# Kernel optimization log

Measured on AMD Instinct MI355X. Metric: run time of the kernel, lower is better.

## Reference

```python
import jax, jax.numpy as jnp
import numpy as np

B, N = 2, 6
FC, FH, FW = 256, 32, 88            # encoder feature shape
ORFH, ORFW = 256, 704               # original image H, W
OUT_C = 128
D_ST, D_END, D_STEP = 1.0, 60.0, 3.0
NXV, NYV, NZV = 256, 256, 1         # BEV voxel grid (x, y, z)
DXV = np.array([0.4, 0.4, 20.0], np.float32)          # dx
BXV = np.array([-51.0, -51.0, 0.0], np.float32)       # bx = bound_lo + dx/2
BN_EPS = 1e-3


def _conv(x, w, b):
    y = jax.lax.conv_general_dilated(x, w, (1, 1), 'SAME',
                                     dimension_numbers=('NCHW', 'OIHW', 'NCHW'))
    return y + b[None, :, None, None]


def _bn(x, scale, bias, mean, var):
    inv = scale / jnp.sqrt(var + BN_EPS)
    return x * inv[None, :, None, None] + (bias - mean * inv)[None, :, None, None]


def _frustum():
    ds = jnp.arange(D_ST, D_END, D_STEP, dtype=jnp.float32)      # (D,)
    xs = jnp.linspace(0.0, ORFW - 1.0, FW)
    ys = jnp.linspace(0.0, ORFH - 1.0, FH)
    f = jnp.stack(jnp.broadcast_arrays(xs[None, None, :], ys[None, :, None],
                                       ds[:, None, None]), axis=-1)  # (D,FH,FW,3)
    return f, ds


def _forward(cam2ego_rot, cam2ego_trans, cam_intrins, post_cam2ego_rot,
             post_cam2ego_trans, img_feats,
             conv1_w, conv1_b, bn1_s, bn1_b, bn1_m, bn1_v,
             conv2_w, conv2_b, bn2_s, bn2_b, bn2_m, bn2_v,
             conv3_w, conv3_b):
    frustum, depth_vals = _frustum()
    D = depth_vals.shape[0]
    # ---- geometry (GaussianLSS.get_geometry) ----
    pts = frustum[None, None] - post_cam2ego_trans[:, :, None, None, None, :]
    inv_post = jnp.linalg.inv(post_cam2ego_rot)                       # (B,N,3,3)
    pts = jnp.einsum('bnij,bndhwj->bndhwi', inv_post, pts)
    pts = jnp.concatenate([pts[..., :2] * pts[..., 2:3], pts[..., 2:3]], -1)
    combine = cam2ego_rot @ jnp.linalg.inv(cam_intrins)
    geometry = (jnp.einsum('bnij,bndhwj->bndhwi', combine, pts)
                + cam2ego_trans[:, :, None, None, None, :])           # (B,N,D,H,W,3)
    # ---- depth net + gaussian depth distribution (get_cam_feature) ----
    x = img_feats.reshape(B * N, FC, FH, FW)
    x = jax.nn.relu(_bn(_conv(x, conv1_w, conv1_b), bn1_s, bn1_b, bn1_m, bn1_v))
    x = jax.nn.relu(_bn(_conv(x, conv2_w, conv2_b), bn2_s, bn2_b, bn2_m, bn2_v))
    x = _conv(x, conv3_w, conv3_b)                                    # (BN, OUT_C+2, H, W)
    mu, log_sigma, feats = x[:, 0], x[:, 1], x[:, 2:]
    sigma = jnp.exp(log_sigma) + 1e-6
    g = jnp.exp(-0.5 * (depth_vals[None, :, None, None] - mu[:, None]) ** 2
                / (sigma[:, None] ** 2))                              # (BN,D,H,W)
    g = g / (jnp.sum(g, axis=1, keepdims=True) + 1e-6)
    vol = g[:, None] * feats[:, :, None]                              # (BN,C,D,H,W)
    vol = vol.reshape(B, N, OUT_C, D, FH, FW).transpose(0, 1, 3, 4, 5, 2)  # (B,N,D,H,W,C)
    # ---- bev_pool: voxelize + scatter-add ----
    dx = jnp.asarray(DXV)
    bx = jnp.asarray(BXV)
    geom = ((geometry - (bx - dx / 2.0)) / dx).astype(jnp.int32)      # trunc like .long()
    gx, gy, gz = geom[..., 0], geom[..., 1], geom[..., 2]
    kept = ((gx >= 0) & (gx < NXV) & (gy >= 0) & (gy < NYV)
            & (gz >= 0) & (gz < NZV))                                 # (B,N,D,H,W)
    bidx = jnp.arange(B, dtype=jnp.int32)[:, None, None, None, None]
    flat = ((bidx * NZV + gz) * NXV + gx) * NYV + gy
    flat = jnp.where(kept, flat, 0)
    w = kept.astype(vol.dtype)
    data = (vol * w[..., None]).reshape(-1, OUT_C)
    bev = jax.ops.segment_sum(data, flat.reshape(-1),
                              num_segments=B * NZV * NXV * NYV)
    # torch: (B,C,Z,X,Y) -> cat(unbind(dim=2), 1) -> (B, Z*C, X, Y)
    bev = bev.reshape(B, NZV, NXV, NYV, OUT_C).transpose(0, 1, 4, 2, 3)
    bev = bev.reshape(B, NZV * OUT_C, NXV, NYV)
    # ---- ref_bev_pool mask ----
    counts = jax.ops.segment_sum(w.reshape(-1), flat.reshape(-1),
                                 num_segments=B * NZV * NXV * NYV)
    mask = jnp.any(counts.reshape(B, NZV, NXV, NYV) > 0, axis=1)      # (B,X,Y) bool
    return bev, mask


def setup_inputs() -> dict:
    key = jax.random.key(0)
    ks = jax.random.split(key, 16)
    # camera->ego rotation: cam z -> ego x, cam x -> -ego y, cam y -> -ego z
    R = jnp.array([[0., 0., 1.], [-1., 0., 0.], [0., -1., 0.]], jnp.float32)
    cam2ego_rot = jnp.tile(R, (B, N, 1, 1)) + 0.01 * jax.random.normal(ks[0], (B, N, 3, 3))
    cam2ego_trans = jax.random.uniform(ks[1], (B, N, 3), minval=-2.0, maxval=2.0)
    K = jnp.array([[500., 0., ORFW / 2.], [0., 500., ORFH / 2.], [0., 0., 1.]], jnp.float32)
    cam_intrins = jnp.tile(K, (B, N, 1, 1))
    post_cam2ego_rot = jnp.tile(jnp.eye(3, dtype=jnp.float32), (B, N, 1, 1)) \
        + 0.005 * jax.random.normal(ks[2], (B, N, 3, 3))
    post_cam2ego_trans = 0.5 * jax.random.normal(ks[3], (B, N, 3))
    img_feats = 0.1 * jax.random.normal(ks[4], (B, N, FC, FH, FW))
    conv3_b = jnp.zeros((OUT_C + 2,)).at[0].set(25.0).at[1].set(2.3)  # mu~25m, sigma~10m
    return dict(
        cam2ego_rot=cam2ego_rot, cam2ego_trans=cam2ego_trans,
        cam_intrins=cam_intrins, post_cam2ego_rot=post_cam2ego_rot,
        post_cam2ego_trans=post_cam2ego_trans, img_feats=img_feats,
        conv1_w=0.02 * jax.random.normal(ks[5], (FC, FC, 3, 3)),
        conv1_b=jnp.zeros((FC,)),
        bn1_s=1.0 + 0.01 * jax.random.normal(ks[6], (FC,)),
        bn1_b=0.01 * jax.random.normal(ks[7], (FC,)),
        bn1_m=0.01 * jax.random.normal(ks[8], (FC,)),
        bn1_v=1.0 + 0.1 * jax.random.uniform(ks[9], (FC,)),
        conv2_w=0.02 * jax.random.normal(ks[10], (FC, FC, 3, 3)),
        conv2_b=jnp.zeros((FC,)),
        bn2_s=1.0 + 0.01 * jax.random.normal(ks[11], (FC,)),
        bn2_b=0.01 * jax.random.normal(ks[12], (FC,)),
        bn2_m=0.01 * jax.random.normal(ks[13], (FC,)),
        bn2_v=1.0 + 0.1 * jax.random.uniform(ks[14], (FC,)),
        conv3_w=0.02 * jax.random.normal(ks[15], (OUT_C + 2, FC, 1, 1)),
        conv3_b=conv3_b,
    )


def reference(cam2ego_rot, cam2ego_trans, cam_intrins, post_cam2ego_rot,
              post_cam2ego_trans, img_feats,
              conv1_w, conv1_b, bn1_s, bn1_b, bn1_m, bn1_v,
              conv2_w, conv2_b, bn2_s, bn2_b, bn2_m, bn2_v,
              conv3_w, conv3_b):
    return _forward(cam2ego_rot, cam2ego_trans, cam_intrins, post_cam2ego_rot,
                    post_cam2ego_trans, img_feats,
                    conv1_w, conv1_b, bn1_s, bn1_b, bn1_m, bn1_v,
                    conv2_w, conv2_b, bn2_s, bn2_b, bn2_m, bn2_v,
                    conv3_w, conv3_b)
```

## Files before the change

kernel.cpp:

```cpp
#include <hip/hip_runtime.h>
#include <math.h>

typedef unsigned short ushort_t;
typedef unsigned int uint_t;

#define NIMG 12
#define NCH  256
#define FH   32
#define FW   88
#define NPIX 2816
#define NDEP 20
#define NOUTC 128
#define NVOX 65536
#define NPTS 675840
#define NKEY 131072
#define BEV_FLOATS 16777216u

#define B_MATS   0u
#define B_A1     4096u
#define B_C1     5120u
#define B_A2     6144u
#define B_C2     7168u
#define B_TOT    278528u
#define B_FEAT   282624u
#define B_RECS   17584128u
#define B_BEV    22990848u
#define B_VCODE  22990848u
#define B_WT     25694208u
#define B_CNT    28397568u
#define B_OFFS   28921856u
#define B_CUR    29446144u
#define B_SPINE  29970432u
#define B_XBF    29972480u
#define B_ACT1   47273984u
#define B_ACT2   64575488u
#define B_WSWZ1  81876992u
#define B_WSWZ2  83056640u
#define B_WSWZ3  84236288u

typedef __attribute__((ext_vector_type(8))) short bf16x8;
typedef __attribute__((ext_vector_type(4))) float floatx4;
typedef __attribute__((ext_vector_type(4))) uint_t u32x4;

__device__ __forceinline__ ushort_t f2bf(float f) {
    uint_t x = __float_as_uint(f);
    return (ushort_t)((x + 0x7fffu + ((x >> 16) & 1u)) >> 16);
}
__device__ __forceinline__ float bf2f(ushort_t u) {
    return __uint_as_float(((uint_t)u) << 16);
}

__device__ __forceinline__ void inv3x3(const float* __restrict__ M, float* __restrict__ o) {
    float a=M[0],b=M[1],c=M[2],d=M[3],e=M[4],f=M[5],g=M[6],h=M[7],i=M[8];
    float A = e*i - f*h;
    float B = c*h - b*i;
    float C = b*f - c*e;
    float D = f*g - d*i;
    float E = a*i - c*g;
    float F = c*d - a*f;
    float G = d*h - e*g;
    float H = b*g - a*h;
    float I = a*e - b*d;
    float det = a*A + b*D + c*G;
    float id = 1.0f / det;
    o[0]=A*id; o[1]=B*id; o[2]=C*id;
    o[3]=D*id; o[4]=E*id; o[5]=F*id;
    o[6]=G*id; o[7]=H*id; o[8]=I*id;
}

__device__ __forceinline__ void wprep_one(
    const float* __restrict__ w, ushort_t* __restrict__ dst,
    int ntap, int ncib, int ncog, int nco, int nci, int idx, bool split)
{
    int j = idx & 7;
    int l = (idx >> 3) & 63;
    int pairidx = idx >> 9;
    int g = pairidx % ncog;
    int b = (pairidx / ncog) % ncib;
    int t = pairidx / (ncog * ncib);
    int co = g * 16 + (l & 15);
    int ci = b * 32 + (l >> 4) * 8 + j;
    float v = 0.0f;
    if (co < nco) v = w[((size_t)co * nci + ci) * ntap + t];
    ushort_t hi = f2bf(v);
    if (split) {
        dst[(size_t)pairidx * 1024 + l * 8 + j]       = hi;
        dst[(size_t)pairidx * 1024 + 512 + l * 8 + j] = f2bf(v - bf2f(hi));
    } else {
        dst[(size_t)pairidx * 512 + l * 8 + j] = hi;
    }
}

__global__ __launch_bounds__(256) void wprep_all_kernel(
    const float* __restrict__ w1, ushort_t* __restrict__ d1,
    const float* __restrict__ w2, ushort_t* __restrict__ d2,
    const float* __restrict__ w3, ushort_t* __restrict__ d3,
    const float* __restrict__ c2e_rot, const float* __restrict__ c2e_trans,
    const float* __restrict__ intrins, const float* __restrict__ post_rot,
    const float* __restrict__ post_trans,
    const float* __restrict__ c1b, const float* __restrict__ s1,
    const float* __restrict__ bb1, const float* __restrict__ m1, const float* __restrict__ v1,
    const float* __restrict__ c2b, const float* __restrict__ s2,
    const float* __restrict__ bb2, const float* __restrict__ m2, const float* __restrict__ v2,
    float* __restrict__ mats, float* __restrict__ A1, float* __restrict__ C1,
    float* __restrict__ A2, float* __restrict__ C2)
{
    int bid = blockIdx.x;
    int t = threadIdx.x;
    if (bid < 2304) {
        wprep_one(w1, d1, 9, 8, 16, 256, 256, bid * 256 + t, false);
    } else if (bid < 4608) {
        wprep_one(w2, d2, 9, 8, 16, 256, 256, (bid - 2304) * 256 + t, false);
    } else if (bid < 4752) {
        int idx = (bid - 4608) * 256 + t;
        if (idx < 36864) wprep_one(w3, d3, 1, 8, 9, 130, 256, idx, true);
    } else {
        if (t < NIMG) {
            float ip[9], ki[9], comb[9];
            inv3x3(post_rot + t*9, ip);
            inv3x3(intrins  + t*9, ki);
            const float* R = c2e_rot + t*9;
            #pragma unroll
            for (int r = 0; r < 3; ++r)
                #pragma unroll
                for (int c = 0; c < 3; ++c)
                    comb[r*3+c] = R[r*3+0]*ki[0*3+c] + R[r*3+1]*ki[1*3+c] + R[r*3+2]*ki[2*3+c];
            float* M = mats + t*24;
            #pragma unroll
            for (int k = 0; k < 9; ++k) { M[k] = ip[k]; M[9+k] = comb[k]; }
            M[18] = c2e_trans[t*3+0]; M[19] = c2e_trans[t*3+1]; M[20] = c2e_trans[t*3+2];
            M[21] = post_trans[t*3+0]; M[22] = post_trans[t*3+1]; M[23] = post_trans[t*3+2];
        }
        float i1 = s1[t] / sqrtf(v1[t] + 1e-3f);
        A1[t] = i1;
        C1[t] = (c1b[t] - m1[t]) * i1 + bb1[t];
        float i2 = s2[t] / sqrtf(v2[t] + 1e-3f);
        A2[t] = i2;
        C2[t] = (c2b[t] - m2[t]) * i2 + bb2[t];
    }
}

__global__ __launch_bounds__(256) void geom_kernel(
    const float* __restrict__ mats, int* __restrict__ vcode, uint_t* __restrict__ cnt)
{
    int i = blockIdx.x * 256 + threadIdx.x;
    int lane = threadIdx.x & 63;
    int hw  = i % NPIX;
    int tmp = i / NPIX;
    int d   = tmp % NDEP;
    int bn  = tmp / NDEP;
    int h = hw / FW, w = hw - h * FW;
    const float* M = mats + bn * 24;
    float xs = (float)w * (703.0f / 87.0f);
    float ys = (float)h * (255.0f / 31.0f);
    float dv = 1.0f + 3.0f * (float)d;
    float fx = xs - M[21], fy = ys - M[22], fz = dv - M[23];
    float p0 = M[0]*fx + M[1]*fy + M[2]*fz;
    float p1 = M[3]*fx + M[4]*fy + M[5]*fz;
    float p2 = M[6]*fx + M[7]*fy + M[8]*fz;
    p0 *= p2; p1 *= p2;
    float gx = M[ 9]*p0 + M[10]*p1 + M[11]*p2 + M[18];
    float gy = M[12]*p0 + M[13]*p1 + M[14]*p2 + M[19];
    float gz = M[15]*p0 + M[16]*p1 + M[17]*p2 + M[20];
    const float cx = -51.0f - 0.2f, cy = -51.0f - 0.2f, cz = 0.0f - 10.0f;
    int ix = (int)((gx - cx) / 0.4f);
    int iy = (int)((gy - cy) / 0.4f);
    int iz = (int)((gz - cz) / 20.0f);
    bool kept = (ix >= 0) && (ix < 256) && (iy >= 0) && (iy < 256) && (iz == 0);
    int code = kept ? ((ix << 8) | iy) : -1;
    vcode[i] = code;

    int b = bn / 6;
    uint_t key = kept ? (uint_t)((b << 16) | code) : 0xFFFFFFFFu;
    uint_t prevkey = __shfl_up(key, 1);
    bool leader = (lane == 0) || (key != prevkey);
    unsigned long long mask = __ballot(leader);
    if (leader && kept) {
        unsigned long long higher = mask & ~((2ULL << lane) - 1ULL);
        int nxt = higher ? (__ffsll((long long)higher) - 1) : 64;
        atomicAdd(&cnt[key], (uint_t)(nxt - lane));
    }
}

__global__ __launch_bounds__(256) void cast_transpose_kernel(
    const float* __restrict__ in, ushort_t* __restrict__ out)
{
    __shared__ __align__(16) ushort_t lds[64 * 264];
    int img = blockIdx.y;
    int px0 = blockIdx.x * 64;
    int t = threadIdx.x;
    const float* src = in + (size_t)img * NCH * NPIX;
    int pxl = t & 63;
    int cib = t >> 6;
    #pragma unroll 4
    for (int cc = 0; cc < 64; ++cc) {
        int ci = cc * 4 + cib;
        float v = src[(size_t)ci * NPIX + px0 + pxl];
        lds[pxl * 264 + ci] = f2bf(v);
    }
    __syncthreads();
    int wv = t >> 6, lane = t & 63;
    uint2* outv = (uint2*)out;
    #pragma unroll
    for (int i = 0; i < 16; ++i) {
        int p = wv * 16 + i;
        uint2 val = *(const uint2*)&lds[p * 264 + lane * 4];
        outv[(size_t)(img * NPIX + px0 + p) * 64 + lane] = val;
    }
}

__global__ __launch_bounds__(256, 3) void conv3x3_mfma(
    const ushort_t* __restrict__ in,
    const ushort_t* __restrict__ wswz,
    const float* __restrict__ Abn, const float* __restrict__ Cbn,
    ushort_t* __restrict__ out)
{
    __shared__ __align__(16) ushort_t lds[2][8640];
    int bx = blockIdx.x;
    int cg = blockIdx.y;
    int img = bx >> 5, h = bx & 31;
    int t = threadIdx.x;
    int w = t >> 6, l = t & 63;
    int q = l >> 4, c = l & 15;
    const int n0s[6] = {0, 16, 32, 48, 64, 72};

    for (int i = t; i < 8640; i += 256) ((uint_t*)lds)[i] = 0;

    const u32x4* src4 = (const u32x4*)(in + (size_t)img * NPIX * 256);
    const bf16x8* wsA = (const bf16x8*)wswz;

    int gbase[5], loff[5];
    bool sval[5];
    #pragma unroll
    for (int k = 0; k < 5; ++k) {
        int p = t + k * 256;
        bool valid = (p < 1056);
        int chunk = p >> 2, sub = p & 3;
        int r = chunk / 88;
        int col = chunk - r * 88;
        int hin = h - 1 + r;
        bool inb = valid && (hin >= 0) && (hin < FH);
        sval[k] = inb;
        gbase[k] = inb ? ((hin * 88 + col) * 32 + sub) : 0;
        int cs = col + 1;
        int slot = sub ^ ((cs >> 1) & 3);
        loff[k] = ((r * 90 + cs) * 4 + slot) * 8;
    }

    floatx4 acc[2][6];
    #pragma unroll
    for (int m = 0; m < 2; ++m)
        #pragma unroll
        for (int n = 0; n < 6; ++n)
            acc[m][n] = (floatx4){0.f, 0.f, 0.f, 0.f};

    int g0 = cg * 8 + w * 2;

    __syncthreads();
    #pragma unroll
    for (int k = 0; k < 5; ++k)
        if (sval[k]) *(u32x4*)&lds[0][loff[k]] = src4[gbase[k]];

    int buf = 0;
    for (int kb = 0; kb < 8; ++kb) {
        __syncthreads();
        u32x4 sreg[5];
        if (kb < 7) {
            #pragma unroll
            for (int k = 0; k < 5; ++k)
                if (sval[k]) sreg[k] = src4[gbase[k] + (kb + 1) * 4];
        }
        const bf16x8* B = (const bf16x8*)lds[buf];

        bf16x8 a0, a1;
        {
            int pa = (0 * 8 + kb) * 16;
            a0 = wsA[(size_t)(pa + g0    ) * 64 + l];
            a1 = wsA[(size_t)(pa + g0 + 1) * 64 + l];
        }
        #pragma unroll
        for (int t9 = 0; t9 < 9; ++t9) {
            bf16x8 na0, na1;
            if (t9 < 8) {
                int pa = ((t9 + 1) * 8 + kb) * 16;
                na0 = wsA[(size_t)(pa + g0    ) * 64 + l];
                na1 = wsA[(size_t)(pa + g0 + 1) * 64 + l];
            }
            int ky = t9 / 3, kx = t9 - ky * 3;
            #pragma unroll
            for (int n = 0; n < 6; ++n) {
                int col = n0s[n] + kx + c;
                int slot = q ^ ((col >> 1) & 3);
                bf16x8 b = B[(ky * 90 + col) * 4 + slot];
                acc[0][n] = __builtin_amdgcn_mfma_f32_16x16x32_bf16(a0, b, acc[0][n], 0, 0, 0);
                acc[1][n] = __builtin_amdgcn_mfma_f32_16x16x32_bf16(a1, b, acc[1][n], 0, 0, 0);
            }
            if (t9 < 8) { a0 = na0; a1 = na1; }
        }
        if (kb < 7) {
            #pragma unroll
            for (int k = 0; k < 5; ++k)
                if (sval[k]) *(u32x4*)&lds[buf ^ 1][loff[k]] = sreg[k];
        }
        buf ^= 1;
    }

    #pragma unroll
    for (int m = 0; m < 2; ++m) {
        int cob = cg * 128 + w * 32 + m * 16 + q * 4;
        float ba0 = Abn[cob+0], ba1 = Abn[cob+1], ba2 = Abn[cob+2], ba3 = Abn[cob+3];
        float bc0 = Cbn[cob+0], bc1 = Cbn[cob+1], bc2 = Cbn[cob+2], bc3 = Cbn[cob+3];
        #pragma unroll
        for (int n = 0; n < 6; ++n) {
            if (n == 5 && c < 8) continue;
            int col = n0s[n] + c;
            floatx4 v = acc[m][n];
            uint_t lo = (uint_t)f2bf(fmaxf(v[0]*ba0+bc0, 0.f)) | ((uint_t)f2bf(fmaxf(v[1]*ba1+bc1, 0.f)) << 16);
            uint_t hi = (uint_t)f2bf(fmaxf(v[2]*ba2+bc2, 0.f)) | ((uint_t)f2bf(fmaxf(v[3]*ba3+bc3, 0.f)) << 16);
            uint2 val; val.x = lo; val.y = hi;
            *(uint2*)&out[((size_t)img * NPIX + h * 88 + col) * 256 + cob] = val;
        }
    }
}

__global__ __launch_bounds__(256, 4) void gemm1x1_mfma(
    const ushort_t* __restrict__ act2,
    const ushort_t* __restrict__ wswz3,
    const float* __restrict__ b3,
    ushort_t* __restrict__ feat, float* __restrict__ wt)
{
    int t = threadIdx.x, wv = t >> 6, l = t & 63, q = l >> 4, c = l & 15;
    int n0 = (blockIdx.x * 4 + wv) * 16;
    int px = n0 + c;
    const bf16x8* A = (const bf16x8*)wswz3;
    const bf16x8* B = (const bf16x8*)act2;
    floatx4 acc[9];
    #pragma unroll
    for (int g = 0; g < 9; ++g) acc[g] = (floatx4){0.f, 0.f, 0.f, 0.f};
    for (int kb = 0; kb < 8; ++kb) {
        bf16x8 b = B[(size_t)px * 32 + kb * 4 + q];
        #pragma unroll
        for (int g = 0; g < 9; ++g) {
            size_t pa = (size_t)(kb * 9 + g) * 128;
            acc[g] = __builtin_amdgcn_mfma_f32_16x16x32_bf16(A[pa + l],      b, acc[g], 0, 0, 0);
            acc[g] = __builtin_amdgcn_mfma_f32_16x16x32_bf16(A[pa + 64 + l], b, acc[g], 0, 0, 0);
        }
    }
    #pragma unroll
    for (int g = 0; g < 9; ++g) {
        #pragma unroll
        for (int r = 0; r < 4; ++r) {
            int co = g * 16 + q * 4 + r;
            if (co < 2 || co >= 130) continue;
            feat[(size_t)px * 128 + (co - 2)] = f2bf(acc[g][r] + b3[co]);
        }
    }
    float muv = acc[0][0] + b3[0];
    float lsv = acc[0][1] + b3[1];
    float mu_b  = __shfl(muv, c);
    float sig   = expf(__shfl(lsv, c)) + 1e-6f;
    float ninv2 = -0.5f / (sig * sig);
    float g5[5]; float s = 0.0f;
    #pragma unroll
    for (int j = 0; j < 5; ++j) {
        float dv = 1.0f + 3.0f * (float)(q * 5 + j);
        float df = dv - mu_b;
        g5[j] = expf(df * df * ninv2);
        s += g5[j];
    }
    s += __shfl_xor(s, 16);
    s += __shfl_xor(s, 32);
    float inv = 1.0f / (s + 1e-6f);
    #pragma unroll
    for (int j = 0; j < 5; ++j)
        wt[(size_t)px * NDEP + q * 5 + j] = g5[j] * inv;
}

__global__ __launch_bounds__(256) void scan_block_kernel(
    const uint_t* __restrict__ cnt, uint_t* __restrict__ offs, uint_t* __restrict__ spine)
{
    __shared__ uint_t s[256];
    int t = threadIdx.x;
    int i = blockIdx.x * 256 + t;
    uint_t v = cnt[i];
    s[t] = v;
    __syncthreads();
    #pragma unroll
    for (int off = 1; off < 256; off <<= 1) {
        uint_t add = (t >= off) ? s[t - off] : 0u;
        __syncthreads();
        s[t] += add;
        __syncthreads();
    }
    offs[i] = s[t] - v;
    if (t == 255) spine[blockIdx.x] = s[255];
}

__global__ __launch_bounds__(256) void fixup_kernel(
    uint_t* __restrict__ offs, const uint_t* __restrict__ spine,
    uint_t* __restrict__ cursor, const uint_t* __restrict__ cnt,
    float* __restrict__ mask_out, uint_t* __restrict__ total)
{
    __shared__ uint_t red[256];
    int bid = blockIdx.x, t = threadIdx.x;
    uint_t part = 0;
    for (int j = t; j < bid; j += 256) part += spine[j];
    red[t] = part;
    __syncthreads();
    #pragma unroll
    for (int off = 128; off > 0; off >>= 1) {
        if (t < off) red[t] += red[t + off];
        __syncthreads();
    }
    uint_t prefix = red[0];
    int i = bid * 256 + t;
    uint_t o = offs[i] + prefix;
    offs[i] = o;
    cursor[i] = o;
    uint_t n = cnt[i];
    mask_out[i] = (n > 0) ? 1.0f : 0.0f;
    if (i == NKEY - 1) *total = o + n;
}

__global__ __launch_bounds__(256) void scatter_kernel(
    const int* __restrict__ vcode, const float* __restrict__ wt,
    uint_t* __restrict__ cursor, uint2* __restrict__ recs)
{
    int i = blockIdx.x * 256 + threadIdx.x;
    int lane = threadIdx.x & 63;
    int code = vcode[i];
    int hw  = i % NPIX;
    int tmp = i / NPIX;
    int d   = tmp % NDEP;
    int bn  = tmp / NDEP;
    int b   = bn / 6;
    int gp  = bn * NPIX + hw;
    bool active = (code >= 0);
    uint_t key = active ? (uint_t)((b << 16) | code) : 0xFFFFFFFFu;
    uint2 r;
    r.x = ((uint_t)(code & 0xffff) << 16) | (uint_t)gp;
    r.y = active ? __float_as_uint(wt[(size_t)gp * NDEP + d]) : 0u;

    uint_t prevkey = __shfl_up(key, 1);
    bool leader = (lane == 0) || (key != prevkey);
    unsigned long long mask = __ballot(leader);
    uint_t base = 0;
    if (leader && active) {
        unsigned long long higher = mask & ~((2ULL << lane) - 1ULL);
        int nxt = higher ? (__ffsll((long long)higher) - 1) : 64;
        base = atomicAdd(&cursor[key], (uint_t)(nxt - lane));
    }
    unsigned long long lower = mask & ((2ULL << lane) - 1ULL);
    int lead = 63 - __clzll((long long)lower);
    base = __shfl(base, lead);
    if (active) recs[base + (lane - lead)] = r;
}

__global__ __launch_bounds__(256) void segreduce_kernel(
    const uint2* __restrict__ recs, const uint_t* __restrict__ total,
    const uint_t* __restrict__ featu,
    float* __restrict__ bev_tmp)
{
    uint_t R = *total;
    int wid = blockIdx.x * 4 + (threadIdx.x >> 6);
    uint_t start = (uint_t)wid * 64u;
    if (start >= R) return;
    int lane = threadIdx.x & 63;
    uint_t ustart = __builtin_amdgcn_readfirstlane(start);

    uint_t myidx = ustart + (uint_t)lane;
    if (myidx >= R) myidx = R - 1u;
    uint2 mr = recs[myidx];

    uint_t rx0 = (uint_t)__shfl((int)mr.x, 0);
    uint_t gp00 = rx0 & 0xffffu;
    uint_t prevk = ((gp00 >= 16896u) ? 0x10000u : 0u) | (rx0 >> 16);
    float acc0 = 0.f, acc1 = 0.f;

    uint_t fbuf[2][16];
    #pragma unroll
    for (int j = 0; j < 16; ++j) {
        uint_t rx = (uint_t)__shfl((int)mr.x, j);
        fbuf[0][j] = featu[(size_t)(rx & 0xffffu) * 64 + lane];
    }
    #pragma unroll
    for (int b = 0; b < 4; ++b) {
        if (b < 3) {
            #pragma unroll
            for (int j = 0; j < 16; ++j) {
                uint_t rx = (uint_t)__shfl((int)mr.x, (b + 1) * 16 + j);
                fbuf[(b + 1) & 1][j] = featu[(size_t)(rx & 0xffffu) * 64 + lane];
            }
        }
        #pragma unroll
        for (int j = 0; j < 16; ++j) {
            int e = b * 16 + j;
            uint_t rx = (uint_t)__shfl((int)mr.x, e);
            uint_t ry = (uint_t)__shfl((int)mr.y, e);
            uint_t gp = rx & 0xffffu;
            uint_t key = ((gp >= 16896u) ? 0x10000u : 0u) | (rx >> 16);
            float wv = __uint_as_float(ry);
            if (ustart + (uint_t)e >= R) { key = prevk; wv = 0.f; }
            if (key != prevk) {
                float* p = bev_tmp + (size_t)prevk * NOUTC;
                atomicAdd(p + 2 * lane,     acc0);
                atomicAdd(p + 2 * lane + 1, acc1);
                acc0 = acc1 = 0.f;
                prevk = key;
            }
            uint_t fv = fbuf[b & 1][j];
            acc0 = fmaf(wv, bf2f((ushort_t)(fv & 0xffffu)), acc0);
            acc1 = fmaf(wv, bf2f((ushort_t)(fv >> 16)),     acc1);
        }
    }
    float* p = bev_tmp + (size_t)prevk * NOUTC;
    atomicAdd(p + 2 * lane,     acc0);
    atomicAdd(p + 2 * lane + 1, acc1);
}

__global__ __launch_bounds__(256) void transpose_kernel(
    const float* __restrict__ bev_tmp, float* __restrict__ bev_out)
{
    __shared__ float lds[64 * 129];
    int blk = blockIdx.x;
    int b   = blk >> 10;
    int v0  = (blk & 1023) * 64;
    int t   = threadIdx.x;
    const float* src = bev_tmp + ((size_t)b * NVOX + v0) * NOUTC;
    #pragma unroll
    for (int k = 0; k < 32; ++k) {
        int idx = k * 256 + t;
        int v = idx >> 7, ch = idx & 127;
        lds[v * 129 + ch] = src[idx];
    }
    __syncthreads();
    float* dst = bev_out + (size_t)b * NOUTC * NVOX + v0;
    #pragma unroll
    for (int k = 0; k < 32; ++k) {
        int idx = k * 256 + t;
        int vl = idx & 63, ch = idx >> 6;
        dst[(size_t)ch * NVOX + vl] = lds[vl * 129 + ch];
    }
}

extern "C" void kernel_launch(void* const* d_in, const int* in_sizes, int n_in,
                              void* d_out, int out_size, void* d_ws, size_t ws_size,
                              hipStream_t stream) {
    const float* c2e_rot    = (const float*)d_in[0];
    const float* c2e_trans  = (const float*)d_in[1];
    const float* intrins    = (const float*)d_in[2];
    const float* post_rot   = (const float*)d_in[3];
    const float* post_trans = (const float*)d_in[4];
    const float* img_feats  = (const float*)d_in[5];
    const float* conv1_w    = (const float*)d_in[6];
    const float* conv1_b    = (const float*)d_in[7];
    const float* bn1_s = (const float*)d_in[8];
    const float* bn1_b = (const float*)d_in[9];
    const float* bn1_m = (const float*)d_in[10];
    const float* bn1_v = (const float*)d_in[11];
    const float* conv2_w = (const float*)d_in[12];
    const float* conv2_b = (const float*)d_in[13];
    const float* bn2_s = (const float*)d_in[14];
    const float* bn2_b = (const float*)d_in[15];
    const float* bn2_m = (const float*)d_in[16];
    const float* bn2_v = (const float*)d_in[17];
    const float* conv3_w = (const float*)d_in[18];
    const float* conv3_b = (const float*)d_in[19];

    char* base = (char*)d_ws;
    float*    mats   = (float*)(base + B_MATS);
    float*    A1     = (float*)(base + B_A1);
    float*    C1     = (float*)(base + B_C1);
    float*    A2     = (float*)(base + B_A2);
    float*    C2     = (float*)(base + B_C2);
    uint_t*   total  = (uint_t*)(base + B_TOT);
    ushort_t* feat   = (ushort_t*)(base + B_FEAT);
    uint2*    recs   = (uint2*)(base + B_RECS);
    float*    bevtmp = (float*)(base + B_BEV);
    int*      vcode  = (int*)(base + B_VCODE);
    float*    wt     = (float*)(base + B_WT);
    uint_t*   cnt    = (uint_t*)(base + B_CNT);
    uint_t*   offs   = (uint_t*)(base + B_OFFS);
    uint_t*   cursor = (uint_t*)(base + B_CUR);
    uint_t*   spine  = (uint_t*)(base + B_SPINE);
    ushort_t* xbf    = (ushort_t*)(base + B_XBF);
    ushort_t* act1   = (ushort_t*)(base + B_ACT1);
    ushort_t* act2   = (ushort_t*)(base + B_ACT2);
    ushort_t* wswz1  = (ushort_t*)(base + B_WSWZ1);
    ushort_t* wswz2  = (ushort_t*)(base + B_WSWZ2);
    ushort_t* wswz3  = (ushort_t*)(base + B_WSWZ3);

    float* bev_out  = (float*)d_out;
    float* mask_out = bev_out + BEV_FLOATS;

    hipMemsetAsync(cnt, 0, NKEY * sizeof(uint_t), stream);
    wprep_all_kernel<<<4753, 256, 0, stream>>>(conv1_w, wswz1, conv2_w, wswz2, conv3_w, wswz3,
                                               c2e_rot, c2e_trans, intrins, post_rot, post_trans,
                                               conv1_b, bn1_s, bn1_b, bn1_m, bn1_v,
                                               conv2_b, bn2_s, bn2_b, bn2_m, bn2_v,
                                               mats, A1, C1, A2, C2);
    geom_kernel<<<NPTS / 256, 256, 0, stream>>>(mats, vcode, cnt);
    cast_transpose_kernel<<<dim3(44, 12), 256, 0, stream>>>(img_feats, xbf);
    conv3x3_mfma<<<dim3(NIMG * 32, 2), 256, 0, stream>>>(xbf,  wswz1, A1, C1, act1);
    conv3x3_mfma<<<dim3(NIMG * 32, 2), 256, 0, stream>>>(act1, wswz2, A2, C2, act2);
    gemm1x1_mfma<<<528, 256, 0, stream>>>(act2, wswz3, conv3_b, feat, wt);
    scan_block_kernel<<<NKEY / 256, 256, 0, stream>>>(cnt, offs, spine);
    fixup_kernel<<<NKEY / 256, 256, 0, stream>>>(offs, spine, cursor, cnt, mask_out, total);
    scatter_kernel<<<NPTS / 256, 256, 0, stream>>>(vcode, wt, cursor, recs);
    hipMemsetAsync(bevtmp, 0, (size_t)BEV_FLOATS * sizeof(float), stream);
    segreduce_kernel<<<(NPTS / 64 + 3) / 4, 256, 0, stream>>>(recs, total, (const uint_t*)feat, bevtmp);
    transpose_kernel<<<2048, 256, 0, stream>>>(bevtmp, bev_out);
}
```

Measured before the change: 359.2 us.

## Fuse geometry and cast-transpose into prep kernel; skip empty BEV tiles in transpose

The separate geometry and cast-transpose launches are merged into the weight-prep kernel as extra block ranges. Each geometry thread now recomputes the per-camera matrix inverses itself instead of reading a precomputed matrix buffer. The fixup kernel also writes a per-64-voxel occupancy byte, and the transpose kernel uses it to write zeros directly for empty tiles instead of reading the temporary BEV buffer. This saves two launches and the reads of the empty BEV region, at the cost of redundant per-thread 3x3 inversions and a larger shared-memory footprint for every prep block.

```diff
diff --git a/kernel.cpp b/kernel.cpp
--- a/kernel.cpp
+++ b/kernel.cpp
@@ -16,7 +16,7 @@
 #define NKEY 131072
 #define BEV_FLOATS 16777216u
 
-#define B_MATS   0u
+#define B_OCC    0u
 #define B_A1     4096u
 #define B_C1     5120u
 #define B_A2     6144u
@@ -38,6 +38,13 @@
 #define B_WSWZ2  83056640u
 #define B_WSWZ3  84236288u
 
+#define PREP_W2    2304
+#define PREP_W3    4608
+#define PREP_BN    4752
+#define PREP_CAST0 4753
+#define PREP_GEOM0 5281
+#define PREP_NBLK  7921
+
 typedef __attribute__((ext_vector_type(8))) short bf16x8;
 typedef __attribute__((ext_vector_type(4))) float floatx4;
 typedef __attribute__((ext_vector_type(4))) uint_t u32x4;
@@ -91,7 +98,7 @@
     }
 }
 
-__global__ __launch_bounds__(256) void wprep_all_kernel(
+__global__ __launch_bounds__(256) void prep_all_kernel(
     const float* __restrict__ w1, ushort_t* __restrict__ d1,
     const float* __restrict__ w2, ushort_t* __restrict__ d2,
     const float* __restrict__ w3, ushort_t* __restrict__ d3,
@@ -102,110 +109,98 @@
     const float* __restrict__ bb1, const float* __restrict__ m1, const float* __restrict__ v1,
     const float* __restrict__ c2b, const float* __restrict__ s2,
     const float* __restrict__ bb2, const float* __restrict__ m2, const float* __restrict__ v2,
-    float* __restrict__ mats, float* __restrict__ A1, float* __restrict__ C1,
-    float* __restrict__ A2, float* __restrict__ C2)
-{
+    float* __restrict__ A1, float* __restrict__ C1,
+    float* __restrict__ A2, float* __restrict__ C2,
+    const float* __restrict__ img_in, ushort_t* __restrict__ xbf_out,
+    int* __restrict__ vcode, uint_t* __restrict__ cnt)
+{
+    __shared__ __align__(16) ushort_t clds[64 * 264];
     int bid = blockIdx.x;
     int t = threadIdx.x;
-    if (bid < 2304) {
+    if (bid < PREP_W2) {
         wprep_one(w1, d1, 9, 8, 16, 256, 256, bid * 256 + t, false);
-    } else if (bid < 4608) {
-        wprep_one(w2, d2, 9, 8, 16, 256, 256, (bid - 2304) * 256 + t, false);
-    } else if (bid < 4752) {
-        int idx = (bid - 4608) * 256 + t;
+    } else if (bid < PREP_W3) {
+        wprep_one(w2, d2, 9, 8, 16, 256, 256, (bid - PREP_W2) * 256 + t, false);
+    } else if (bid < PREP_BN) {
+        int idx = (bid - PREP_W3) * 256 + t;
         if (idx < 36864) wprep_one(w3, d3, 1, 8, 9, 130, 256, idx, true);
-    } else {
-        if (t < NIMG) {
-            float ip[9], ki[9], comb[9];
-            inv3x3(post_rot + t*9, ip);
-            inv3x3(intrins  + t*9, ki);
-            const float* R = c2e_rot + t*9;
-            #pragma unroll
-            for (int r = 0; r < 3; ++r)
-                #pragma unroll
-                for (int c = 0; c < 3; ++c)
-                    comb[r*3+c] = R[r*3+0]*ki[0*3+c] + R[r*3+1]*ki[1*3+c] + R[r*3+2]*ki[2*3+c];
-            float* M = mats + t*24;
-            #pragma unroll
-            for (int k = 0; k < 9; ++k) { M[k] = ip[k]; M[9+k] = comb[k]; }
-            M[18] = c2e_trans[t*3+0]; M[19] = c2e_trans[t*3+1]; M[20] = c2e_trans[t*3+2];
-            M[21] = post_trans[t*3+0]; M[22] = post_trans[t*3+1]; M[23] = post_trans[t*3+2];
-        }
+    } else if (bid == PREP_BN) {
         float i1 = s1[t] / sqrtf(v1[t] + 1e-3f);
         A1[t] = i1;
         C1[t] = (c1b[t] - m1[t]) * i1 + bb1[t];
         float i2 = s2[t] / sqrtf(v2[t] + 1e-3f);
         A2[t] = i2;
         C2[t] = (c2b[t] - m2[t]) * i2 + bb2[t];
-    }
-}
-
-__global__ __launch_bounds__(256) void geom_kernel(
-    const float* __restrict__ mats, int* __restrict__ vcode, uint_t* __restrict__ cnt)
-{
-    int i = blockIdx.x * 256 + threadIdx.x;
-    int lane = threadIdx.x & 63;
-    int hw  = i % NPIX;
-    int tmp = i / NPIX;
-    int d   = tmp % NDEP;
-    int bn  = tmp / NDEP;
-    int h = hw / FW, w = hw - h * FW;
-    const float* M = mats + bn * 24;
-    float xs = (float)w * (703.0f / 87.0f);
-    float ys = (float)h * (255.0f / 31.0f);
-    float dv = 1.0f + 3.0f * (float)d;
-    float fx = xs - M[21], fy = ys - M[22], fz = dv - M[23];
-    float p0 = M[0]*fx + M[1]*fy + M[2]*fz;
-    float p1 = M[3]*fx + M[4]*fy + M[5]*fz;
-    float p2 = M[6]*fx + M[7]*fy + M[8]*fz;
-    p0 *= p2; p1 *= p2;
-    float gx = M[ 9]*p0 + M[10]*p1 + M[11]*p2 + M[18];
-    float gy = M[12]*p0 + M[13]*p1 + M[14]*p2 + M[19];
-    float gz = M[15]*p0 + M[16]*p1 + M[17]*p2 + M[20];
-    const float cx = -51.0f - 0.2f, cy = -51.0f - 0.2f, cz = 0.0f - 10.0f;
-    int ix = (int)((gx - cx) / 0.4f);
-    int iy = (int)((gy - cy) / 0.4f);
-    int iz = (int)((gz - cz) / 20.0f);
-    bool kept = (ix >= 0) && (ix < 256) && (iy >= 0) && (iy < 256) && (iz == 0);
-    int code = kept ? ((ix << 8) | iy) : -1;
-    vcode[i] = code;
-
-    int b = bn / 6;
-    uint_t key = kept ? (uint_t)((b << 16) | code) : 0xFFFFFFFFu;
-    uint_t prevkey = __shfl_up(key, 1);
-    bool leader = (lane == 0) || (key != prevkey);
-    unsigned long long mask = __ballot(leader);
-    if (leader && kept) {
-        unsigned long long higher = mask & ~((2ULL << lane) - 1ULL);
-        int nxt = higher ? (__ffsll((long long)higher) - 1) : 64;
-        atomicAdd(&cnt[key], (uint_t)(nxt - lane));
-    }
-}
-
-__global__ __launch_bounds__(256) void cast_transpose_kernel(
-    const float* __restrict__ in, ushort_t* __restrict__ out)
-{
-    __shared__ __align__(16) ushort_t lds[64 * 264];
-    int img = blockIdx.y;
-    int px0 = blockIdx.x * 64;
-    int t = threadIdx.x;
-    const float* src = in + (size_t)img * NCH * NPIX;
-    int pxl = t & 63;
-    int cib = t >> 6;
-    #pragma unroll 4
-    for (int cc = 0; cc < 64; ++cc) {
-        int ci = cc * 4 + cib;
-        float v = src[(size_t)ci * NPIX + px0 + pxl];
-        lds[pxl * 264 + ci] = f2bf(v);
-    }
-    __syncthreads();
-    int wv = t >> 6, lane = t & 63;
-    uint2* outv = (uint2*)out;
-    #pragma unroll
-    for (int i = 0; i < 16; ++i) {
-        int p = wv * 16 + i;
-        uint2 val = *(const uint2*)&lds[p * 264 + lane * 4];
-        outv[(size_t)(img * NPIX + px0 + p) * 64 + lane] = val;
+    } else if (bid < PREP_GEOM0) {
+        int cblk = bid - PREP_CAST0;
+        int img = cblk / 44;
+        int px0 = (cblk - img * 44) * 64;
+        const float* src = img_in + (size_t)img * NCH * NPIX;
+        int pxl = t & 63;
+        int cib = t >> 6;
+        #pragma unroll 4
+        for (int cc = 0; cc < 64; ++cc) {
+            int ci = cc * 4 + cib;
+            float v = src[(size_t)ci * NPIX + px0 + pxl];
+            clds[pxl * 264 + ci] = f2bf(v);
+        }
+        __syncthreads();
+        int wv = t >> 6, lane = t & 63;
+        uint2* outv = (uint2*)xbf_out;
+        #pragma unroll
+        for (int i = 0; i < 16; ++i) {
+            int p = wv * 16 + i;
+            uint2 val = *(const uint2*)&clds[p * 264 + lane * 4];
+            outv[(size_t)(img * NPIX + px0 + p) * 64 + lane] = val;
+        }
+    } else {
+        int i = (bid - PREP_GEOM0) * 256 + t;
+        int lane = t & 63;
+        int hw  = i % NPIX;
+        int tmp = i / NPIX;
+        int d   = tmp % NDEP;
+        int bn  = tmp / NDEP;
+        int h = hw / FW, w = hw - h * FW;
+        float ip[9], ki[9], comb[9];
+        inv3x3(post_rot + bn * 9, ip);
+        inv3x3(intrins  + bn * 9, ki);
+        const float* R = c2e_rot + bn * 9;
+        #pragma unroll
+        for (int r = 0; r < 3; ++r)
+            #pragma unroll
+            for (int cc = 0; cc < 3; ++cc)
+                comb[r*3+cc] = R[r*3+0]*ki[0*3+cc] + R[r*3+1]*ki[1*3+cc] + R[r*3+2]*ki[2*3+cc];
+        float xs = (float)w * (703.0f / 87.0f);
+        float ys = (float)h * (255.0f / 31.0f);
+        float dv = 1.0f + 3.0f * (float)d;
+        float fx = xs - post_trans[bn*3+0];
+        float fy = ys - post_trans[bn*3+1];
+        float fz = dv - post_trans[bn*3+2];
+        float p0 = ip[0]*fx + ip[1]*fy + ip[2]*fz;
+        float p1 = ip[3]*fx + ip[4]*fy + ip[5]*fz;
+        float p2 = ip[6]*fx + ip[7]*fy + ip[8]*fz;
+        p0 *= p2; p1 *= p2;
+        float gx = comb[0]*p0 + comb[1]*p1 + comb[2]*p2 + c2e_trans[bn*3+0];
+        float gy = comb[3]*p0 + comb[4]*p1 + comb[5]*p2 + c2e_trans[bn*3+1];
+        float gz = comb[6]*p0 + comb[7]*p1 + comb[8]*p2 + c2e_trans[bn*3+2];
+        const float cx = -51.0f - 0.2f, cy = -51.0f - 0.2f, cz = 0.0f - 10.0f;
+        int ix = (int)((gx - cx) / 0.4f);
+        int iy = (int)((gy - cy) / 0.4f);
+        int iz = (int)((gz - cz) / 20.0f);
+        bool kept = (ix >= 0) && (ix < 256) && (iy >= 0) && (iy < 256) && (iz == 0);
+        int code = kept ? ((ix << 8) | iy) : -1;
+        vcode[i] = code;
+
+        int b = bn / 6;
+        uint_t key = kept ? (uint_t)((b << 16) | code) : 0xFFFFFFFFu;
+        uint_t prevkey = __shfl_up(key, 1);
+        bool leader = (lane == 0) || (key != prevkey);
+        unsigned long long mask = __ballot(leader);
+        if (leader && kept) {
+            unsigned long long higher = mask & ~((2ULL << lane) - 1ULL);
+            int nxt = higher ? (__ffsll((long long)higher) - 1) : 64;
+            atomicAdd(&cnt[key], (uint_t)(nxt - lane));
+        }
     }
 }
 
@@ -399,7 +394,8 @@
 __global__ __launch_bounds__(256) void fixup_kernel(
     uint_t* __restrict__ offs, const uint_t* __restrict__ spine,
     uint_t* __restrict__ cursor, const uint_t* __restrict__ cnt,
-    float* __restrict__ mask_out, uint_t* __restrict__ total)
+    float* __restrict__ mask_out, uint_t* __restrict__ total,
+    unsigned char* __restrict__ occ)
 {
     __shared__ uint_t red[256];
     int bid = blockIdx.x, t = threadIdx.x;
@@ -419,6 +415,9 @@
     cursor[i] = o;
     uint_t n = cnt[i];
     mask_out[i] = (n > 0) ? 1.0f : 0.0f;
+    int lane = t & 63, wv = t >> 6;
+    unsigned long long any = __ballot(n > 0u);
+    if (lane == 0) occ[bid * 4 + wv] = any ? 1 : 0;
     if (i == NKEY - 1) *total = o + n;
 }
 
@@ -519,13 +518,24 @@
 }
 
 __global__ __launch_bounds__(256) void transpose_kernel(
-    const float* __restrict__ bev_tmp, float* __restrict__ bev_out)
+    const float* __restrict__ bev_tmp, const unsigned char* __restrict__ occ,
+    float* __restrict__ bev_out)
 {
     __shared__ float lds[64 * 129];
     int blk = blockIdx.x;
     int b   = blk >> 10;
     int v0  = (blk & 1023) * 64;
     int t   = threadIdx.x;
+    float* dst = bev_out + (size_t)b * NOUTC * NVOX + v0;
+    if (!occ[blk]) {
+        #pragma unroll
+        for (int k = 0; k < 32; ++k) {
+            int idx = k * 256 + t;
+            int vl = idx & 63, ch = idx >> 6;
+            dst[(size_t)ch * NVOX + vl] = 0.0f;
+        }
+        return;
+    }
     const float* src = bev_tmp + ((size_t)b * NVOX + v0) * NOUTC;
     #pragma unroll
     for (int k = 0; k < 32; ++k) {
@@ -534,7 +544,6 @@
         lds[v * 129 + ch] = src[idx];
     }
     __syncthreads();
-    float* dst = bev_out + (size_t)b * NOUTC * NVOX + v0;
     #pragma unroll
     for (int k = 0; k < 32; ++k) {
         int idx = k * 256 + t;
@@ -568,7 +577,7 @@
     const float* conv3_b = (const float*)d_in[19];
 
     char* base = (char*)d_ws;
-    float*    mats   = (float*)(base + B_MATS);
+    unsigned char* occ = (unsigned char*)(base + B_OCC);
     float*    A1     = (float*)(base + B_A1);
     float*    C1     = (float*)(base + B_C1);
     float*    A2     = (float*)(base + B_A2);
@@ -594,20 +603,20 @@
     float* mask_out = bev_out + BEV_FLOATS;
 
     hipMemsetAsync(cnt, 0, NKEY * sizeof(uint_t), stream);
-    wprep_all_kernel<<<4753, 256, 0, stream>>>(conv1_w, wswz1, conv2_w, wswz2, conv3_w, wswz3,
-                                               c2e_rot, c2e_trans, intrins, post_rot, post_trans,
-                                               conv1_b, bn1_s, bn1_b, bn1_m, bn1_v,
-                                               conv2_b, bn2_s, bn2_b, bn2_m, bn2_v,
-                                               mats, A1, C1, A2, C2);
-    geom_kernel<<<NPTS / 256, 256, 0, stream>>>(mats, vcode, cnt);
-    cast_transpose_kernel<<<dim3(44, 12), 256, 0, stream>>>(img_feats, xbf);
+    prep_all_kernel<<<PREP_NBLK, 256, 0, stream>>>(
+        conv1_w, wswz1, conv2_w, wswz2, conv3_w, wswz3,
+        c2e_rot, c2e_trans, intrins, post_rot, post_trans,
+        conv1_b, bn1_s, bn1_b, bn1_m, bn1_v,
+        conv2_b, bn2_s, bn2_b, bn2_m, bn2_v,
+        A1, C1, A2, C2,
+        img_feats, xbf, vcode, cnt);
     conv3x3_mfma<<<dim3(NIMG * 32, 2), 256, 0, stream>>>(xbf,  wswz1, A1, C1, act1);
     conv3x3_mfma<<<dim3(NIMG * 32, 2), 256, 0, stream>>>(act1, wswz2, A2, C2, act2);
     gemm1x1_mfma<<<528, 256, 0, stream>>>(act2, wswz3, conv3_b, feat, wt);
     scan_block_kernel<<<NKEY / 256, 256, 0, stream>>>(cnt, offs, spine);
-    fixup_kernel<<<NKEY / 256, 256, 0, stream>>>(offs, spine, cursor, cnt, mask_out, total);
+    fixup_kernel<<<NKEY / 256, 256, 0, stream>>>(offs, spine, cursor, cnt, mask_out, total, occ);
     scatter_kernel<<<NPTS / 256, 256, 0, stream>>>(vcode, wt, cursor, recs);
     hipMemsetAsync(bevtmp, 0, (size_t)BEV_FLOATS * sizeof(float), stream);
     segreduce_kernel<<<(NPTS / 64 + 3) / 4, 256, 0, stream>>>(recs, total, (const uint_t*)feat, bevtmp);
-    transpose_kernel<<<2048, 256, 0, stream>>>(bevtmp, bev_out);
-}
+    transpose_kernel<<<2048, 256, 0, stream>>>(bevtmp, occ, bev_out);
+}
```

New measurement: 351.0 us. -2.3%, faster.
